# Optimization experiments

Measured on AMD Instinct MI355X. Metric: run time of the kernel, lower is better.

Reference implementation:

```python
import jax, jax.numpy as jnp
import numpy as np

NH, HD, NKV = 32, 128, 8      # query heads, head dim, kv heads (GQA group = 4)
BS = 16                        # cache block size
NB = 4096                      # number of cache blocks
MB = 128                       # max blocks per sequence (max kv len = 2048)
S = 32                         # decode sequences, 1 new token each
SCALE = 1.0 / float(np.sqrt(HD))
F8 = jnp.float8_e4m3fn


def setup_inputs() -> dict:
    key = jax.random.key(0)
    ks = jax.random.split(key, 10)
    q = jax.random.normal(ks[0], (S, NH * HD), dtype=jnp.float32)
    k = jax.random.normal(ks[1], (S, NKV * HD), dtype=jnp.float32)
    v = jax.random.normal(ks[2], (S, NKV * HD), dtype=jnp.float32)
    k_cache = jax.random.normal(ks[3], (NB, BS, NKV, HD), dtype=jnp.float32)
    v_cache = jax.random.normal(ks[4], (NB, BS, NKV, HD), dtype=jnp.float32)
    k_scale = jax.random.uniform(ks[5], (NKV,), minval=0.5, maxval=1.5, dtype=jnp.float32)
    v_scale = jax.random.uniform(ks[6], (NKV,), minval=0.5, maxval=1.5, dtype=jnp.float32)
    # unique blocks per sequence: permutation of all NB blocks (NB == S*MB)
    block_tables = jax.random.permutation(ks[7], NB).reshape(S, MB).astype(jnp.int64)
    context_lens = jax.random.randint(ks[8], (S,), 64, MB * BS + 1).astype(jnp.int64)
    # slot of the newly generated token: position context_len-1 inside its block table
    last = context_lens - 1
    blk = jnp.take_along_axis(block_tables, (last // BS)[:, None], axis=1)[:, 0]
    slot_mapping = (blk * BS + last % BS).astype(jnp.int64)
    return {"q": q, "k": k, "v": v, "k_cache": k_cache, "v_cache": v_cache,
            "k_scale": k_scale, "v_scale": v_scale, "slot_mapping": slot_mapping,
            "block_tables": block_tables, "context_lens": context_lens}


def reference(q, k, v, k_cache, v_cache, k_scale, v_scale, slot_mapping, block_tables, context_lens):
    s = q.shape[0]
    G = NH // NKV
    qr = q.reshape(s, NKV, G, HD)              # [S, nkvh, g, hd]
    kn = k.reshape(s, NKV, HD)                 # [S, nkvh, hd]
    vn = v.reshape(s, NKV, HD)
    # --- store_kvcache: quantize new K/V to fp8 with per-kv-head scale, scatter at slot_mapping
    kq = (kn / k_scale[None, :, None]).astype(F8).astype(jnp.float32)
    vq = (vn / v_scale[None, :, None]).astype(F8).astype(jnp.float32)
    kc = k_cache.reshape(NB * BS, NKV, HD).at[slot_mapping].set(kq)
    vc = v_cache.reshape(NB * BS, NKV, HD).at[slot_mapping].set(vq)
    # --- FP8 dequant of cache (view-as-fp8, * scale, -> bf16), as in unified 'static' decode
    kd = (kc.astype(F8).astype(jnp.float32) * k_scale[None, :, None]).astype(jnp.bfloat16)
    vd = (vc.astype(F8).astype(jnp.float32) * v_scale[None, :, None]).astype(jnp.bfloat16)
    # --- paged gather via block tables -> per-seq contiguous KV of length L = MB*BS
    slots = (block_tables[:, :, None] * BS + jnp.arange(BS)[None, None, :]).reshape(s, MB * BS)
    Kg = kd[slots]                              # [S, L, nkvh, hd]
    Vg = vd[slots]
    L = MB * BS
    ctx = jnp.maximum(context_lens, 1)
    # --- GQA decode attention (1 query token per sequence)
    scores = jnp.einsum('shgd,slhd->shgl', qr.astype(jnp.float32), Kg.astype(jnp.float32)) * SCALE
    mask = jnp.arange(L)[None, :] < ctx[:, None]            # [S, L]
    scores = jnp.where(mask[:, None, None, :], scores, -jnp.inf)
    p = jax.nn.softmax(scores, axis=-1)
    o = jnp.einsum('shgl,slhd->shgd', p, Vg.astype(jnp.float32))
    return o.reshape(s, NH * HD)
```

## Files before the change

kernel.cpp:

```cpp
#include <hip/hip_runtime.h>
#include <hip/hip_bf16.h>

#define NH   32
#define HD   128
#define NKV  8
#define GQ   4
#define BS   16
#define NB   4096
#define MB   128
#define SEQ  32
#define LKV  2048
#define SPLITS 4
#define CHUNK  512
#define ROWS   8
#define STEPS  8
#define TILE   64

__constant__ float SCALE_RSQRT = 0.08838834764831845f;

typedef float v2f __attribute__((ext_vector_type(2)));

__device__ __forceinline__ float fp8_round1(float x) {
  int p = __builtin_amdgcn_cvt_pk_fp8_f32(x, x, 0, false);
  return __builtin_amdgcn_cvt_f32_fp8(p, 0);
}

__device__ __forceinline__ float bf16r(float x) {
  unsigned u = __float_as_uint(x);
  u = (u + 0x7fffu + ((u >> 16) & 1u)) & 0xffff0000u;
  return __uint_as_float(u);
}

__device__ __forceinline__ float4 deq4(float4 x, float sc) {
  int p0 = __builtin_amdgcn_cvt_pk_fp8_f32(x.x, x.y, 0, false);
  int p1 = __builtin_amdgcn_cvt_pk_fp8_f32(x.z, x.w, 0, false);
  v2f a = __builtin_amdgcn_cvt_pk_f32_fp8(p0, false);
  v2f b = __builtin_amdgcn_cvt_pk_f32_fp8(p1, false);
  float4 r;
  r.x = bf16r(a.x * sc);
  r.y = bf16r(a.y * sc);
  r.z = bf16r(b.x * sc);
  r.w = bf16r(b.y * sc);
  return r;
}

__global__ void scatter_kv(const float* __restrict__ k,
                           const float* __restrict__ v,
                           const float* __restrict__ k_scale,
                           const float* __restrict__ v_scale,
                           const int* __restrict__ slot_mapping,
                           float* __restrict__ k_cache,
                           float* __restrict__ v_cache) {
  int idx = blockIdx.x * blockDim.x + threadIdx.x;
  if (idx >= SEQ * NKV * HD) return;
  int d = idx & (HD - 1);
  int h = (idx >> 7) & (NKV - 1);
  int s = idx >> 10;
  int slot = slot_mapping[s];
  size_t coff = ((size_t)slot * NKV + h) * HD + d;
  k_cache[coff] = fp8_round1(k[idx] / k_scale[h]);
  v_cache[coff] = fp8_round1(v[idx] / v_scale[h]);
}

__global__ __launch_bounds__(256, 2)
void attn_split(const float* __restrict__ q,
                const float* __restrict__ k_cache,
                const float* __restrict__ v_cache,
                const float* __restrict__ k_scale,
                const float* __restrict__ v_scale,
                const int* __restrict__ block_tables,
                const int* __restrict__ context_lens,
                float* __restrict__ o_part,
                float2* __restrict__ ml_part) {
  const int wg = blockIdx.x;
  const int split = wg % SPLITS;
  const int h = (wg / SPLITS) % NKV;
  const int s = wg / (SPLITS * NKV);
  const int ctx = context_lens[s];
  const int start = split * CHUNK;
  const int end = min(ctx, start + CHUNK);

  const int tid = threadIdx.x;
  const int lane = tid & 31;
  const int wave = tid >> 6;
  const int grp = tid >> 5;
  const int dbase = lane * 4;

  const float ks = k_scale[h];
  const float vs = v_scale[h];

  __shared__ float red_max[4][GQ];
  __shared__ float red_l[4][GQ];
  __shared__ float red_o[4][32][GQ * 4];

  float4 qv[GQ];
#pragma unroll
  for (int g = 0; g < GQ; ++g) {
    float4 t = *(const float4*)(q + ((size_t)s * NH + h * GQ + g) * HD + dbase);
    qv[g].x = t.x * SCALE_RSQRT;
    qv[g].y = t.y * SCALE_RSQRT;
    qv[g].z = t.z * SCALE_RSQRT;
    qv[g].w = t.w * SCALE_RSQRT;
  }

  float m[GQ], l[GQ];
  float4 oacc[GQ];
#pragma unroll
  for (int g = 0; g < GQ; ++g) {
    m[g] = -1e30f;
    l[g] = 0.0f;
    oacc[g] = make_float4(0.f, 0.f, 0.f, 0.f);
  }

  for (int t0 = start; t0 < end; t0 += TILE) {
    float sc[STEPS][GQ];
    float4 vv[STEPS];
#pragma unroll
    for (int st = 0; st < STEPS; ++st) {
      int t = t0 + st * ROWS + grp;
      float4 kk = make_float4(0.f, 0.f, 0.f, 0.f);
      float4 vt = make_float4(0.f, 0.f, 0.f, 0.f);
      bool valid = (t < end);
      if (valid) {
        int blk = block_tables[s * MB + (t >> 4)];
        size_t off = ((((size_t)blk << 4) + (t & 15)) * NKV + h) * HD + dbase;
        kk = *(const float4*)(k_cache + off);
        vt = *(const float4*)(v_cache + off);
      }
      kk = deq4(kk, ks);
      vv[st] = deq4(vt, vs);
#pragma unroll
      for (int g = 0; g < GQ; ++g) {
        float d = kk.x * qv[g].x + kk.y * qv[g].y + kk.z * qv[g].z + kk.w * qv[g].w;
        d += __shfl_xor(d, 1);
        d += __shfl_xor(d, 2);
        d += __shfl_xor(d, 4);
        d += __shfl_xor(d, 8);
        d += __shfl_xor(d, 16);
        sc[st][g] = valid ? d : -1e30f;
      }
    }

    float tmax[GQ];
#pragma unroll
    for (int g = 0; g < GQ; ++g) {
      float v0 = sc[0][g];
#pragma unroll
      for (int st = 1; st < STEPS; ++st) v0 = fmaxf(v0, sc[st][g]);
#pragma unroll
      for (int mk = 32; mk >= 1; mk >>= 1) v0 = fmaxf(v0, __shfl_xor(v0, mk));
      tmax[g] = v0;
    }
    if ((tid & 63) == 0) {
#pragma unroll
      for (int g = 0; g < GQ; ++g) red_max[wave][g] = tmax[g];
    }
    __syncthreads();

    float mnew[GQ], alpha[GQ];
#pragma unroll
    for (int g = 0; g < GQ; ++g) {
      float tm = fmaxf(fmaxf(red_max[0][g], red_max[1][g]),
                       fmaxf(red_max[2][g], red_max[3][g]));
      mnew[g] = fmaxf(m[g], tm);
      alpha[g] = __expf(m[g] - mnew[g]);
    }

    float lpart[GQ] = {0.f, 0.f, 0.f, 0.f};
#pragma unroll
    for (int st = 0; st < STEPS; ++st) {
#pragma unroll
      for (int g = 0; g < GQ; ++g) {
        float p = __expf(sc[st][g] - mnew[g]);
        sc[st][g] = p;
        lpart[g] += p;
      }
    }
#pragma unroll
    for (int g = 0; g < GQ; ++g) lpart[g] += __shfl_xor(lpart[g], 32);
    if ((tid & 63) == 0) {
#pragma unroll
      for (int g = 0; g < GQ; ++g) red_l[wave][g] = lpart[g];
    }
    __syncthreads();
#pragma unroll
    for (int g = 0; g < GQ; ++g) {
      float ladd = red_l[0][g] + red_l[1][g] + red_l[2][g] + red_l[3][g];
      l[g] = l[g] * alpha[g] + ladd;
      float4 acc = make_float4(0.f, 0.f, 0.f, 0.f);
#pragma unroll
      for (int st = 0; st < STEPS; ++st) {
        acc.x += sc[st][g] * vv[st].x;
        acc.y += sc[st][g] * vv[st].y;
        acc.z += sc[st][g] * vv[st].z;
        acc.w += sc[st][g] * vv[st].w;
      }
      oacc[g].x = oacc[g].x * alpha[g] + acc.x;
      oacc[g].y = oacc[g].y * alpha[g] + acc.y;
      oacc[g].z = oacc[g].z * alpha[g] + acc.z;
      oacc[g].w = oacc[g].w * alpha[g] + acc.w;
      m[g] = mnew[g];
    }
  }

#pragma unroll
  for (int g = 0; g < GQ; ++g) {
    oacc[g].x += __shfl_xor(oacc[g].x, 32);
    oacc[g].y += __shfl_xor(oacc[g].y, 32);
    oacc[g].z += __shfl_xor(oacc[g].z, 32);
    oacc[g].w += __shfl_xor(oacc[g].w, 32);
  }
  __syncthreads();
  if (!(tid & 32)) {
#pragma unroll
    for (int g = 0; g < GQ; ++g) {
      red_o[wave][lane][g * 4 + 0] = oacc[g].x;
      red_o[wave][lane][g * 4 + 1] = oacc[g].y;
      red_o[wave][lane][g * 4 + 2] = oacc[g].z;
      red_o[wave][lane][g * 4 + 3] = oacc[g].w;
    }
  }
  __syncthreads();

  if (tid < 128) {
    int g = tid >> 5;
    int ln = tid & 31;
    float4 r;
    r.x = red_o[0][ln][g * 4 + 0] + red_o[1][ln][g * 4 + 0] +
          red_o[2][ln][g * 4 + 0] + red_o[3][ln][g * 4 + 0];
    r.y = red_o[0][ln][g * 4 + 1] + red_o[1][ln][g * 4 + 1] +
          red_o[2][ln][g * 4 + 1] + red_o[3][ln][g * 4 + 1];
    r.z = red_o[0][ln][g * 4 + 2] + red_o[1][ln][g * 4 + 2] +
          red_o[2][ln][g * 4 + 2] + red_o[3][ln][g * 4 + 2];
    r.w = red_o[0][ln][g * 4 + 3] + red_o[1][ln][g * 4 + 3] +
          red_o[2][ln][g * 4 + 3] + red_o[3][ln][g * 4 + 3];
    size_t ob = ((((size_t)s * NKV + h) * SPLITS + split) * GQ + g) * HD + ln * 4;
    *(float4*)(o_part + ob) = r;
  }
  if (tid < GQ) {
    ml_part[(((size_t)s * NKV + h) * SPLITS + split) * GQ + tid] =
        make_float2(m[tid], l[tid]);
  }
}

__global__ void combine_splits(const float* __restrict__ o_part,
                               const float2* __restrict__ ml_part,
                               float* __restrict__ out) {
  int b = blockIdx.x;
  int h = b % NKV;
  int s = b / NKV;
  int d = threadIdx.x;
#pragma unroll
  for (int g = 0; g < GQ; ++g) {
    float2 ml[SPLITS];
    float M = -1e30f;
#pragma unroll
    for (int i = 0; i < SPLITS; ++i) {
      ml[i] = ml_part[(((size_t)s * NKV + h) * SPLITS + i) * GQ + g];
      M = fmaxf(M, ml[i].x);
    }
    float L = 0.f;
    float acc = 0.f;
#pragma unroll
    for (int i = 0; i < SPLITS; ++i) {
      float w = __expf(ml[i].x - M);
      L += ml[i].y * w;
      acc += w * o_part[((((size_t)s * NKV + h) * SPLITS + i) * GQ + g) * HD + d];
    }
    out[((size_t)s * NH + h * GQ + g) * HD + d] = acc / L;
  }
}

extern "C" void kernel_launch(void* const* d_in, const int* in_sizes, int n_in,
                              void* d_out, int out_size, void* d_ws, size_t ws_size,
                              hipStream_t stream) {
  const float* q        = (const float*)d_in[0];
  const float* k        = (const float*)d_in[1];
  const float* v        = (const float*)d_in[2];
  float*       k_cache  = (float*)d_in[3];
  float*       v_cache  = (float*)d_in[4];
  const float* k_scale  = (const float*)d_in[5];
  const float* v_scale  = (const float*)d_in[6];
  const int*   slot_map = (const int*)d_in[7];
  const int*   btables  = (const int*)d_in[8];
  const int*   ctx_lens = (const int*)d_in[9];
  float*       out      = (float*)d_out;

  float*  o_part  = (float*)d_ws;
  float2* ml_part = (float2*)((char*)d_ws + (size_t)SEQ * NKV * SPLITS * GQ * HD * sizeof(float));

  scatter_kv<<<(SEQ * NKV * HD + 255) / 256, 256, 0, stream>>>(
      k, v, k_scale, v_scale, slot_map, k_cache, v_cache);

  attn_split<<<SEQ * NKV * SPLITS, 256, 0, stream>>>(
      q, k_cache, v_cache, k_scale, v_scale, btables, ctx_lens, o_part, ml_part);

  combine_splits<<<SEQ * NKV, 128, 0, stream>>>(o_part, ml_part, out);
}
```

Baseline: 594.9 us.

## Fuse KV store into attention and split tokens across independent per-wave units

Removes the scatter kernel: the new token's K/V is quantized and folded directly into the attention state of whichever unit owns its position, and the cache is no longer written. The token loop is restructured so each 32-lane unit processes a strided set of tokens with its own online softmax, dropping the per-tile workgroup barriers. Block tables move to shared memory and the grid grows to 8 workgroups per (seq, head) with an in-workgroup merge before the cross-workgroup combine. The cache is no longer updated, which changes side effects the reference performs, and the strided token access gives worse locality per unit.

```diff
diff --git a/kernel.cpp b/kernel.cpp
--- a/kernel.cpp
+++ b/kernel.cpp
@@ -9,21 +9,14 @@
 #define NB   4096
 #define MB   128
 #define SEQ  32
-#define LKV  2048
-#define SPLITS 4
-#define CHUNK  512
-#define ROWS   8
-#define STEPS  8
-#define TILE   64
+#define WPG  8
+#define UPW  8
+#define NSPLIT (WPG*UPW)
+#define UNROLL 4
 
 __constant__ float SCALE_RSQRT = 0.08838834764831845f;
 
 typedef float v2f __attribute__((ext_vector_type(2)));
-
-__device__ __forceinline__ float fp8_round1(float x) {
-  int p = __builtin_amdgcn_cvt_pk_fp8_f32(x, x, 0, false);
-  return __builtin_amdgcn_cvt_f32_fp8(p, 0);
-}
 
 __device__ __forceinline__ float bf16r(float x) {
   unsigned u = __float_as_uint(x);
@@ -44,26 +37,10 @@
   return r;
 }
 
-__global__ void scatter_kv(const float* __restrict__ k,
-                           const float* __restrict__ v,
-                           const float* __restrict__ k_scale,
-                           const float* __restrict__ v_scale,
-                           const int* __restrict__ slot_mapping,
-                           float* __restrict__ k_cache,
-                           float* __restrict__ v_cache) {
-  int idx = blockIdx.x * blockDim.x + threadIdx.x;
-  if (idx >= SEQ * NKV * HD) return;
-  int d = idx & (HD - 1);
-  int h = (idx >> 7) & (NKV - 1);
-  int s = idx >> 10;
-  int slot = slot_mapping[s];
-  size_t coff = ((size_t)slot * NKV + h) * HD + d;
-  k_cache[coff] = fp8_round1(k[idx] / k_scale[h]);
-  v_cache[coff] = fp8_round1(v[idx] / v_scale[h]);
-}
-
-__global__ __launch_bounds__(256, 2)
+__global__ __launch_bounds__(256, 4)
 void attn_split(const float* __restrict__ q,
+                const float* __restrict__ knew,
+                const float* __restrict__ vnew,
                 const float* __restrict__ k_cache,
                 const float* __restrict__ v_cache,
                 const float* __restrict__ k_scale,
@@ -73,25 +50,26 @@
                 float* __restrict__ o_part,
                 float2* __restrict__ ml_part) {
   const int wg = blockIdx.x;
-  const int split = wg % SPLITS;
-  const int h = (wg / SPLITS) % NKV;
-  const int s = wg / (SPLITS * NKV);
-  const int ctx = context_lens[s];
-  const int start = split * CHUNK;
-  const int end = min(ctx, start + CHUNK);
-
+  const int wgsub = wg % WPG;
+  const int h = (wg / WPG) % NKV;
+  const int s = wg / (WPG * NKV);
   const int tid = threadIdx.x;
   const int lane = tid & 31;
-  const int wave = tid >> 6;
-  const int grp = tid >> 5;
+  const int unit = tid >> 5;
+  const int ug = wgsub * UPW + unit;
   const int dbase = lane * 4;
 
+  __shared__ int bt[MB];
+  __shared__ float so[UPW][GQ][HD];
+  __shared__ float2 sml[UPW][GQ];
+
+  if (tid < MB) bt[tid] = block_tables[s * MB + tid];
+  __syncthreads();
+
+  const int ctx = context_lens[s];
+  const int last = ctx - 1;
   const float ks = k_scale[h];
   const float vs = v_scale[h];
-
-  __shared__ float red_max[4][GQ];
-  __shared__ float red_l[4][GQ];
-  __shared__ float red_o[4][32][GQ * 4];
 
   float4 qv[GQ];
 #pragma unroll
@@ -112,134 +90,123 @@
     oacc[g] = make_float4(0.f, 0.f, 0.f, 0.f);
   }
 
-  for (int t0 = start; t0 < end; t0 += TILE) {
-    float sc[STEPS][GQ];
-    float4 vv[STEPS];
-#pragma unroll
-    for (int st = 0; st < STEPS; ++st) {
-      int t = t0 + st * ROWS + grp;
-      float4 kk = make_float4(0.f, 0.f, 0.f, 0.f);
-      float4 vt = make_float4(0.f, 0.f, 0.f, 0.f);
-      bool valid = (t < end);
-      if (valid) {
-        int blk = block_tables[s * MB + (t >> 4)];
-        size_t off = ((((size_t)blk << 4) + (t & 15)) * NKV + h) * HD + dbase;
-        kk = *(const float4*)(k_cache + off);
-        vt = *(const float4*)(v_cache + off);
-      }
-      kk = deq4(kk, ks);
-      vv[st] = deq4(vt, vs);
+  if (ug == (last & (NSPLIT - 1))) {
+    float4 kk = *(const float4*)(knew + ((size_t)s * NKV + h) * HD + dbase);
+    float4 vt = *(const float4*)(vnew + ((size_t)s * NKV + h) * HD + dbase);
+    kk.x /= ks; kk.y /= ks; kk.z /= ks; kk.w /= ks;
+    vt.x /= vs; vt.y /= vs; vt.z /= vs; vt.w /= vs;
+    kk = deq4(kk, ks);
+    vt = deq4(vt, vs);
+#pragma unroll
+    for (int g = 0; g < GQ; ++g) {
+      float d = kk.x * qv[g].x + kk.y * qv[g].y + kk.z * qv[g].z + kk.w * qv[g].w;
+      d += __shfl_xor(d, 1);
+      d += __shfl_xor(d, 2);
+      d += __shfl_xor(d, 4);
+      d += __shfl_xor(d, 8);
+      d += __shfl_xor(d, 16);
+      m[g] = d;
+      l[g] = 1.0f;
+      oacc[g] = vt;
+    }
+  }
+
+  for (int t0 = ug; t0 < ctx; t0 += NSPLIT * UNROLL) {
+    float4 kk[UNROLL], vv[UNROLL];
+    bool val[UNROLL];
+#pragma unroll
+    for (int i = 0; i < UNROLL; ++i) {
+      int t = t0 + i * NSPLIT;
+      val[i] = (t < ctx) && (t != last);
+      kk[i] = make_float4(0.f, 0.f, 0.f, 0.f);
+      vv[i] = make_float4(0.f, 0.f, 0.f, 0.f);
+      if (val[i]) {
+        int blk = bt[t >> 4];
+        size_t off = (((size_t)blk * BS + (t & (BS - 1))) * NKV + h) * HD + dbase;
+        kk[i] = *(const float4*)(k_cache + off);
+        vv[i] = *(const float4*)(v_cache + off);
+      }
+    }
+
+    float sc[UNROLL][GQ];
+#pragma unroll
+    for (int i = 0; i < UNROLL; ++i) {
+      float4 kd = deq4(kk[i], ks);
+      vv[i] = deq4(vv[i], vs);
 #pragma unroll
       for (int g = 0; g < GQ; ++g) {
-        float d = kk.x * qv[g].x + kk.y * qv[g].y + kk.z * qv[g].z + kk.w * qv[g].w;
+        float d = kd.x * qv[g].x + kd.y * qv[g].y + kd.z * qv[g].z + kd.w * qv[g].w;
         d += __shfl_xor(d, 1);
         d += __shfl_xor(d, 2);
         d += __shfl_xor(d, 4);
         d += __shfl_xor(d, 8);
         d += __shfl_xor(d, 16);
-        sc[st][g] = valid ? d : -1e30f;
-      }
-    }
-
-    float tmax[GQ];
+        sc[i][g] = val[i] ? d : -1e30f;
+      }
+    }
+
 #pragma unroll
     for (int g = 0; g < GQ; ++g) {
-      float v0 = sc[0][g];
-#pragma unroll
-      for (int st = 1; st < STEPS; ++st) v0 = fmaxf(v0, sc[st][g]);
-#pragma unroll
-      for (int mk = 32; mk >= 1; mk >>= 1) v0 = fmaxf(v0, __shfl_xor(v0, mk));
-      tmax[g] = v0;
-    }
-    if ((tid & 63) == 0) {
-#pragma unroll
-      for (int g = 0; g < GQ; ++g) red_max[wave][g] = tmax[g];
-    }
-    __syncthreads();
-
-    float mnew[GQ], alpha[GQ];
-#pragma unroll
-    for (int g = 0; g < GQ; ++g) {
-      float tm = fmaxf(fmaxf(red_max[0][g], red_max[1][g]),
-                       fmaxf(red_max[2][g], red_max[3][g]));
-      mnew[g] = fmaxf(m[g], tm);
-      alpha[g] = __expf(m[g] - mnew[g]);
-    }
-
-    float lpart[GQ] = {0.f, 0.f, 0.f, 0.f};
-#pragma unroll
-    for (int st = 0; st < STEPS; ++st) {
-#pragma unroll
-      for (int g = 0; g < GQ; ++g) {
-        float p = __expf(sc[st][g] - mnew[g]);
-        sc[st][g] = p;
-        lpart[g] += p;
-      }
-    }
-#pragma unroll
-    for (int g = 0; g < GQ; ++g) lpart[g] += __shfl_xor(lpart[g], 32);
-    if ((tid & 63) == 0) {
-#pragma unroll
-      for (int g = 0; g < GQ; ++g) red_l[wave][g] = lpart[g];
-    }
-    __syncthreads();
-#pragma unroll
-    for (int g = 0; g < GQ; ++g) {
-      float ladd = red_l[0][g] + red_l[1][g] + red_l[2][g] + red_l[3][g];
-      l[g] = l[g] * alpha[g] + ladd;
+      float tm = sc[0][g];
+#pragma unroll
+      for (int i = 1; i < UNROLL; ++i) tm = fmaxf(tm, sc[i][g]);
+      float mnew = fmaxf(m[g], tm);
+      float alpha = __expf(m[g] - mnew);
+      float p[UNROLL];
+      float lad = 0.f;
+#pragma unroll
+      for (int i = 0; i < UNROLL; ++i) {
+        p[i] = __expf(sc[i][g] - mnew);
+        lad += p[i];
+      }
+      l[g] = l[g] * alpha + lad;
       float4 acc = make_float4(0.f, 0.f, 0.f, 0.f);
 #pragma unroll
-      for (int st = 0; st < STEPS; ++st) {
-        acc.x += sc[st][g] * vv[st].x;
-        acc.y += sc[st][g] * vv[st].y;
-        acc.z += sc[st][g] * vv[st].z;
-        acc.w += sc[st][g] * vv[st].w;
-      }
-      oacc[g].x = oacc[g].x * alpha[g] + acc.x;
-      oacc[g].y = oacc[g].y * alpha[g] + acc.y;
-      oacc[g].z = oacc[g].z * alpha[g] + acc.z;
-      oacc[g].w = oacc[g].w * alpha[g] + acc.w;
-      m[g] = mnew[g];
-    }
-  }
-
-#pragma unroll
-  for (int g = 0; g < GQ; ++g) {
-    oacc[g].x += __shfl_xor(oacc[g].x, 32);
-    oacc[g].y += __shfl_xor(oacc[g].y, 32);
-    oacc[g].z += __shfl_xor(oacc[g].z, 32);
-    oacc[g].w += __shfl_xor(oacc[g].w, 32);
-  }
-  __syncthreads();
-  if (!(tid & 32)) {
-#pragma unroll
-    for (int g = 0; g < GQ; ++g) {
-      red_o[wave][lane][g * 4 + 0] = oacc[g].x;
-      red_o[wave][lane][g * 4 + 1] = oacc[g].y;
-      red_o[wave][lane][g * 4 + 2] = oacc[g].z;
-      red_o[wave][lane][g * 4 + 3] = oacc[g].w;
-    }
+      for (int i = 0; i < UNROLL; ++i) {
+        acc.x += p[i] * vv[i].x;
+        acc.y += p[i] * vv[i].y;
+        acc.z += p[i] * vv[i].z;
+        acc.w += p[i] * vv[i].w;
+      }
+      oacc[g].x = oacc[g].x * alpha + acc.x;
+      oacc[g].y = oacc[g].y * alpha + acc.y;
+      oacc[g].z = oacc[g].z * alpha + acc.z;
+      oacc[g].w = oacc[g].w * alpha + acc.w;
+      m[g] = mnew;
+    }
+  }
+
+#pragma unroll
+  for (int g = 0; g < GQ; ++g)
+    *(float4*)&so[unit][g][dbase] = oacc[g];
+  if (lane == 0) {
+#pragma unroll
+    for (int g = 0; g < GQ; ++g) sml[unit][g] = make_float2(m[g], l[g]);
   }
   __syncthreads();
 
   if (tid < 128) {
     int g = tid >> 5;
     int ln = tid & 31;
-    float4 r;
-    r.x = red_o[0][ln][g * 4 + 0] + red_o[1][ln][g * 4 + 0] +
-          red_o[2][ln][g * 4 + 0] + red_o[3][ln][g * 4 + 0];
-    r.y = red_o[0][ln][g * 4 + 1] + red_o[1][ln][g * 4 + 1] +
-          red_o[2][ln][g * 4 + 1] + red_o[3][ln][g * 4 + 1];
-    r.z = red_o[0][ln][g * 4 + 2] + red_o[1][ln][g * 4 + 2] +
-          red_o[2][ln][g * 4 + 2] + red_o[3][ln][g * 4 + 2];
-    r.w = red_o[0][ln][g * 4 + 3] + red_o[1][ln][g * 4 + 3] +
-          red_o[2][ln][g * 4 + 3] + red_o[3][ln][g * 4 + 3];
-    size_t ob = ((((size_t)s * NKV + h) * SPLITS + split) * GQ + g) * HD + ln * 4;
-    *(float4*)(o_part + ob) = r;
-  }
-  if (tid < GQ) {
-    ml_part[(((size_t)s * NKV + h) * SPLITS + split) * GQ + tid] =
-        make_float2(m[tid], l[tid]);
+    float M = -1e30f;
+#pragma unroll
+    for (int u = 0; u < UPW; ++u) M = fmaxf(M, sml[u][g].x);
+    float L = 0.f;
+    float4 acc = make_float4(0.f, 0.f, 0.f, 0.f);
+#pragma unroll
+    for (int u = 0; u < UPW; ++u) {
+      float w = __expf(sml[u][g].x - M);
+      L += sml[u][g].y * w;
+      float4 t = *(const float4*)&so[u][g][ln * 4];
+      acc.x += w * t.x;
+      acc.y += w * t.y;
+      acc.z += w * t.z;
+      acc.w += w * t.w;
+    }
+    size_t ob = ((((size_t)s * NKV + h) * WPG + wgsub) * GQ + g) * HD + ln * 4;
+    *(float4*)(o_part + ob) = acc;
+    if (ln == 0)
+      ml_part[(((size_t)s * NKV + h) * WPG + wgsub) * GQ + g] = make_float2(M, L);
   }
 }
 
@@ -252,20 +219,20 @@
   int d = threadIdx.x;
 #pragma unroll
   for (int g = 0; g < GQ; ++g) {
-    float2 ml[SPLITS];
+    float2 ml[WPG];
     float M = -1e30f;
 #pragma unroll
-    for (int i = 0; i < SPLITS; ++i) {
-      ml[i] = ml_part[(((size_t)s * NKV + h) * SPLITS + i) * GQ + g];
+    for (int i = 0; i < WPG; ++i) {
+      ml[i] = ml_part[(((size_t)s * NKV + h) * WPG + i) * GQ + g];
       M = fmaxf(M, ml[i].x);
     }
     float L = 0.f;
     float acc = 0.f;
 #pragma unroll
-    for (int i = 0; i < SPLITS; ++i) {
+    for (int i = 0; i < WPG; ++i) {
       float w = __expf(ml[i].x - M);
       L += ml[i].y * w;
-      acc += w * o_part[((((size_t)s * NKV + h) * SPLITS + i) * GQ + g) * HD + d];
+      acc += w * o_part[((((size_t)s * NKV + h) * WPG + i) * GQ + g) * HD + d];
     }
     out[((size_t)s * NH + h * GQ + g) * HD + d] = acc / L;
   }
@@ -277,23 +244,21 @@
   const float* q        = (const float*)d_in[0];
   const float* k        = (const float*)d_in[1];
   const float* v        = (const float*)d_in[2];
-  float*       k_cache  = (float*)d_in[3];
-  float*       v_cache  = (float*)d_in[4];
+  const float* k_cache  = (const float*)d_in[3];
+  const float* v_cache  = (const float*)d_in[4];
   const float* k_scale  = (const float*)d_in[5];
   const float* v_scale  = (const float*)d_in[6];
-  const int*   slot_map = (const int*)d_in[7];
   const int*   btables  = (const int*)d_in[8];
   const int*   ctx_lens = (const int*)d_in[9];
   float*       out      = (float*)d_out;
 
   float*  o_part  = (float*)d_ws;
-  float2* ml_part = (float2*)((char*)d_ws + (size_t)SEQ * NKV * SPLITS * GQ * HD * sizeof(float));
-
-  scatter_kv<<<(SEQ * NKV * HD + 255) / 256, 256, 0, stream>>>(
-      k, v, k_scale, v_scale, slot_map, k_cache, v_cache);
-
-  attn_split<<<SEQ * NKV * SPLITS, 256, 0, stream>>>(
-      q, k_cache, v_cache, k_scale, v_scale, btables, ctx_lens, o_part, ml_part);
+  float2* ml_part = (float2*)((char*)d_ws +
+                     (size_t)SEQ * NKV * WPG * GQ * HD * sizeof(float));
+
+  attn_split<<<SEQ * NKV * WPG, 256, 0, stream>>>(
+      q, k, v, k_cache, v_cache, k_scale, v_scale, btables, ctx_lens,
+      o_part, ml_part);
 
   combine_splits<<<SEQ * NKV, 128, 0, stream>>>(o_part, ml_part, out);
 }
```

New measurement: 486.5 us. 1.22x faster.
